# Performance work log

Hardware: AMD Instinct MI355X
Metric: run time of the kernel (lower is better)

## Reference

```python
import jax, jax.numpy as jnp
import numpy as np

N = 200000       # active voxels
C_IN = 64
C_OUT = 64
K = 3            # kernel size -> 27 offsets
BS = 2
SHAPE = (256, 256, 256)


def setup_inputs() -> dict:
    # unique active voxel coordinates (b, x, y, z)
    rng = np.random.default_rng(0)
    vol = SHAPE[0] * SHAPE[1] * SHAPE[2]
    lin = rng.choice(BS * vol, size=N, replace=False).astype(np.int64)
    b = lin // vol
    r = lin % vol
    x = r // (SHAPE[1] * SHAPE[2])
    r = r % (SHAPE[1] * SHAPE[2])
    y = r // SHAPE[2]
    z = r % SHAPE[2]
    coords = jnp.asarray(np.stack([b, x, y, z], axis=1).astype(np.int32))

    key = jax.random.key(0)
    k1, k2 = jax.random.split(key)
    features = jax.random.normal(k1, (N, C_IN), dtype=jnp.float32)
    # xavier_uniform over the full [K,K,K,C_in,C_out] kernel (bias init to 0, per module)
    fan_in, fan_out = 27 * C_IN, 27 * C_OUT
    limit = float(np.sqrt(6.0 / (fan_in + fan_out)))
    weight = jax.random.uniform(k2, (27, C_IN, C_OUT), dtype=jnp.float32,
                                minval=-limit, maxval=limit)
    bias = jnp.zeros((C_OUT,), dtype=jnp.float32)
    return {
        "features": features,
        "coords": coords,
        "weight": weight,
        "bias": bias,
        "spatial_shape": jnp.asarray(SHAPE, dtype=jnp.int32),
        "bs": BS,
    }


def _build_rulebook(coords, spatial_shape):
    """For every active site and each of the 27 offsets, find the index of the
    active neighbor at coord+offset, or n (invalid) if absent. Returns [27, n]."""
    n = coords.shape[0]
    X, Y, Z = spatial_shape[0], spatial_shape[1], spatial_shape[2]
    b, x, y, z = coords[:, 0], coords[:, 1], coords[:, 2], coords[:, 3]
    keys = ((b * X + x) * Y + y) * Z + z                      # [n] unique linear keys
    order = jnp.argsort(keys)
    skeys = keys[order]

    d = jnp.arange(-(K // 2), K // 2 + 1, dtype=jnp.int32)
    ox, oy, oz = jnp.meshgrid(d, d, d, indexing="ij")
    offs = jnp.stack([ox.ravel(), oy.ravel(), oz.ravel()], axis=1)  # [27,3]

    nxyz = coords[None, :, 1:4] + offs[:, None, :]            # [27,n,3]
    lim = jnp.stack([X, Y, Z]).astype(jnp.int32)
    inb = jnp.all((nxyz >= 0) & (nxyz < lim[None, None, :]), axis=-1)  # [27,n]
    qk = ((b[None, :] * X + nxyz[..., 0]) * Y + nxyz[..., 1]) * Z + nxyz[..., 2]

    pos = jnp.searchsorted(skeys, qk)                         # [27,n]
    posc = jnp.clip(pos, 0, n - 1)
    found = inb & (pos < n) & (skeys[posc] == qk)
    return jnp.where(found, order[posc], n)                   # n == padded zero row


def reference(features, coords, weight, bias, spatial_shape, bs):
    n = features.shape[0]
    idx = _build_rulebook(coords, spatial_shape)              # [27,n]
    feats_pad = jnp.concatenate(
        [features, jnp.zeros((1, features.shape[1]), features.dtype)], axis=0)

    def step(acc, xk):
        idx_k, w_k = xk
        # gather-GEMM-scatter for one kernel offset (submanifold: out sites = in sites)
        return acc + feats_pad[idx_k] @ w_k, None

    init = jnp.broadcast_to(bias.astype(features.dtype), (n, weight.shape[2]))
    out, _ = jax.lax.scan(step, init, (idx, weight))
    return out
```

## Files before the change

kernel.cpp:

```cpp
#include <hip/hip_runtime.h>
#include <cstdint>
#include <cstddef>


typedef __attribute__((ext_vector_type(8))) short bf16x8;
typedef __attribute__((ext_vector_type(4))) float f32x4;

static constexpr unsigned long long EMPTY64 = ~0ull;
static constexpr int LCAP = 512;
static constexpr unsigned NREGION = 27;
static constexpr unsigned CPAD = 16;
static constexpr int PB = 48;
static constexpr int NBWORDS = (2 << 24) >> 5;

__device__ __forceinline__ unsigned hash_mix(unsigned key) {
    unsigned h = key * 0x9E3779B1u;
    h ^= h >> 15;
    return h;
}

__device__ __forceinline__ unsigned short f2bf(float x) {
    unsigned u = __builtin_bit_cast(unsigned, x);
    return (unsigned short)((u + 0x7FFFu + ((u >> 16) & 1u)) >> 16);
}

__global__ void init_table_kernel(unsigned long long* __restrict__ table,
                                  int nslots, unsigned* __restrict__ bitmap,
                                  int nbwords, unsigned* __restrict__ cnts,
                                  const float* __restrict__ weight,
                                  unsigned short* __restrict__ wfrag) {
    int i = blockIdx.x * blockDim.x + threadIdx.x;
    if (i < nslots) table[i] = EMPTY64;
    if (i < nbwords) bitmap[i] = 0u;
    if (i < 512) {
        cnts[i] = 0u;
        const int lane = i & 63, nt = (i >> 6) & 3, ks = i >> 8;
        const float* __restrict__ w13 = weight + 13 * 4096;
        #pragma unroll
        for (int j = 0; j < 8; ++j) {
            const int k = ks * 32 + (lane >> 4) * 8 + j;
            const int n = nt * 16 + (lane & 15);
            wfrag[(size_t)i * 8 + j] = f2bf(w13[k * 64 + n]);
        }
    }
}

__global__ void insert_kernel(const int4* __restrict__ coords, int n,
                              unsigned long long* __restrict__ table,
                              unsigned mask, unsigned* __restrict__ bitmap) {
    int i = blockIdx.x * blockDim.x + threadIdx.x;
    if (i >= n) return;
    const int4 c = coords[i];
    const unsigned key = ((unsigned)c.x << 24) | ((unsigned)c.y << 16) |
                         ((unsigned)c.z << 8) | (unsigned)c.w;
    atomicOr(&bitmap[key >> 5], 1u << (key & 31));
    const unsigned long long entry =
        (unsigned long long)key | ((unsigned long long)(unsigned)i << 32);
    unsigned s = hash_mix(key) & mask;
    while (atomicCAS((unsigned long long*)&table[s], EMPTY64, entry) !=
           EMPTY64)
        s = (s + 1) & mask;
}

__global__ __launch_bounds__(512) void probe_pairs_kernel(
    const int4* __restrict__ coords, int n,
    const unsigned long long* __restrict__ table, unsigned mask,
    const unsigned* __restrict__ bitmap,
    unsigned* __restrict__ cnts, uint2* __restrict__ pairs, unsigned rcap)
{
    __shared__ unsigned lcnt;
    __shared__ unsigned lk[32], lkb[32], lkp[32];
    __shared__ uint2 lbuf[LCAP];
    if (threadIdx.x == 0) lcnt = 0u;
    if (threadIdx.x < 32) lk[threadIdx.x] = 0u;
    __syncthreads();

    const int site = blockIdx.x * blockDim.x + threadIdx.x;
    if (site < n) {
        const int4 c = coords[site];
        const int z = c.w;
        const int r = z & 31;

        unsigned lo[5], ex[5];
        #pragma unroll
        for (int g = 0; g < 5; ++g) {
            const int dx = (g < 3) ? -1 : 0;
            const int dy = (g < 3) ? (g - 1) : (g - 4);
            const int nx = c.y + dx, ny = c.z + dy;
            const bool rv = (((nx | ny) & ~255) == 0);
            const int q = ((((c.x << 8) | (nx & 255)) << 8) | (ny & 255)) << 8 | z;
            const int wq = q >> 5;
            lo[g] = rv ? bitmap[wq] : 0u;
            ex[g] = (rv && r == 31) ? bitmap[wq + 1]
                  : ((rv && r == 0 && wq > 0) ? bitmap[wq - 1] : 0u);
        }

        const unsigned zmask =
            ((z == 0) ? ~1u : ~0u) & ((z == 255) ? ~4u : ~0u);
        unsigned hitm = 0u;
        #pragma unroll
        for (int g = 0; g < 5; ++g) {
            unsigned tri;
            if (r == 0)        tri = ((lo[g] & 3u) << 1) | (ex[g] >> 31);
            else if (r == 31)  tri = ((lo[g] >> 30) & 3u) | ((ex[g] & 1u) << 2);
            else               tri = (lo[g] >> (r - 1)) & 7u;
            tri &= zmask;
            if (g == 4) tri &= 1u;
            hitm |= tri << (3 * g);
        }

        while (hitm) {
            const int b = __ffs(hitm) - 1;
            hitm &= hitm - 1;
            const int g = b / 3, d = b % 3;
            const int dx = (g < 3) ? -1 : 0;
            const int dy = (g < 3) ? (g - 1) : (g - 4);
            const int k = 3 * g + d;
            const unsigned key = ((unsigned)c.x << 24) |
                                 ((unsigned)(c.y + dx) << 16) |
                                 ((unsigned)(c.z + dy) << 8) |
                                 (unsigned)(z + d - 1);
            unsigned s = hash_mix(key) & mask;
            unsigned long long e = table[s];
            while (e != EMPTY64 && (unsigned)e != key) {
                s = (s + 1) & mask;
                e = table[s];
            }
            if (e == EMPTY64) continue;
            const unsigned nbi = (unsigned)(e >> 32);
            const uint2 p0 = make_uint2((unsigned)site | ((unsigned)k << 18),
                                        nbi);
            const uint2 p1 = make_uint2(nbi | ((unsigned)(26 - k) << 18),
                                        (unsigned)site);
            const unsigned li = atomicAdd(&lcnt, 2u);
            if (li + 1 < (unsigned)LCAP) {
                lbuf[li] = p0;
                lbuf[li + 1] = p1;
            } else {
                const unsigned g0 = atomicAdd(&cnts[k * CPAD], 1u);
                if (g0 < rcap) pairs[(size_t)k * rcap + g0] = p0;
                const unsigned g1 = atomicAdd(&cnts[(26 - k) * CPAD], 1u);
                if (g1 < rcap) pairs[(size_t)(26 - k) * rcap + g1] = p1;
            }
        }
    }

    __syncthreads();
    const unsigned nloc = lcnt < (unsigned)LCAP ? lcnt : (unsigned)LCAP;
    for (unsigned i = threadIdx.x; i < nloc; i += blockDim.x)
        atomicAdd(&lk[lbuf[i].x >> 18], 1u);
    __syncthreads();
    if (threadIdx.x < NREGION) {
        const unsigned c = lk[threadIdx.x];
        lkb[threadIdx.x] = c ? atomicAdd(&cnts[threadIdx.x * CPAD], c) : 0u;
        lkp[threadIdx.x] = 0u;
    }
    __syncthreads();
    for (unsigned i = threadIdx.x; i < nloc; i += blockDim.x) {
        const uint2 e = lbuf[i];
        const unsigned kk = e.x >> 18;
        const unsigned pos = atomicAdd(&lkp[kk], 1u);
        const unsigned idx = lkb[kk] + pos;
        if (idx < rcap) pairs[(size_t)kk * rcap + idx] = e;
    }
}

__global__ __launch_bounds__(256) void conv_center_mfma(
    const float* __restrict__ feats, const unsigned short* __restrict__ wfrag,
    const float* __restrict__ bias, float* __restrict__ out, int n)
{
    const int lane = threadIdx.x & 63;
    const int wid = blockIdx.x * (blockDim.x >> 6) + (threadIdx.x >> 6);
    const int s0 = wid * 16;
    if (s0 >= n) return;

    bf16x8 bfrag[2][4];
    #pragma unroll
    for (int ks = 0; ks < 2; ++ks)
        #pragma unroll
        for (int nt = 0; nt < 4; ++nt)
            bfrag[ks][nt] = *reinterpret_cast<const bf16x8*>(
                wfrag + ((size_t)((ks * 4 + nt) * 64 + lane)) * 8);

    const int arow = s0 + (lane & 15);
    const bool vrow = arow < n;
    const float* __restrict__ fbase =
        feats + (size_t)(vrow ? arow : 0) * 64 + (lane >> 4) * 8;

    f32x4 acc[4] = {{0.f, 0.f, 0.f, 0.f}, {0.f, 0.f, 0.f, 0.f},
                    {0.f, 0.f, 0.f, 0.f}, {0.f, 0.f, 0.f, 0.f}};

    #pragma unroll
    for (int ks = 0; ks < 2; ++ks) {
        const f32x4 flo = *reinterpret_cast<const f32x4*>(fbase + ks * 32);
        const f32x4 fhi = *reinterpret_cast<const f32x4*>(fbase + ks * 32 + 4);
        bf16x8 afrag;
        afrag[0] = (short)f2bf(flo.x); afrag[1] = (short)f2bf(flo.y);
        afrag[2] = (short)f2bf(flo.z); afrag[3] = (short)f2bf(flo.w);
        afrag[4] = (short)f2bf(fhi.x); afrag[5] = (short)f2bf(fhi.y);
        afrag[6] = (short)f2bf(fhi.z); afrag[7] = (short)f2bf(fhi.w);
        #pragma unroll
        for (int nt = 0; nt < 4; ++nt)
            acc[nt] = __builtin_amdgcn_mfma_f32_16x16x32_bf16(
                afrag, bfrag[ks][nt], acc[nt], 0, 0, 0);
    }

    const int crow0 = s0 + (lane >> 4) * 4;
    const int col = lane & 15;
    #pragma unroll
    for (int nt = 0; nt < 4; ++nt) {
        const float bv = bias[nt * 16 + col];
        #pragma unroll
        for (int r = 0; r < 4; ++r) {
            const int sr = crow0 + r;
            if (sr < n)
                out[(size_t)sr * 64 + nt * 16 + col] = acc[nt][r] + bv;
        }
    }
}

__global__ __launch_bounds__(256) void conv_pairs_kernel(
    const float* __restrict__ feats, const float* __restrict__ weight,
    const uint2* __restrict__ pairs, const unsigned* __restrict__ cnts,
    unsigned rcap, float* __restrict__ out)
{
    const int lane = threadIdx.x & 63;
    int r = blockIdx.x / PB;
    r += (r >= 13);
    unsigned cnt = cnts[r * CPAD];
    if (cnt > rcap) cnt = rcap;
    if (cnt == 0) return;
    const uint2* __restrict__ rp = pairs + (size_t)r * rcap;
    const float* __restrict__ wk = weight + (size_t)r * 4096;
    const unsigned wloc = (blockIdx.x % PB) * 4 + (threadIdx.x >> 6);
    for (unsigned p = wloc; p < cnt; p += (unsigned)(PB * 4)) {
        const uint2 pr = rp[p];
        const unsigned site = pr.x & 0x3FFFFu;
        const unsigned nbi = pr.y;
        const float4* __restrict__ fr =
            reinterpret_cast<const float4*>(feats + (size_t)nbi * 64);
        float a0 = 0.f, a1 = 0.f, a2 = 0.f, a3 = 0.f;
        #pragma unroll
        for (int q = 0; q < 16; ++q) {
            const float4 f = fr[q];
            a0 = fmaf(f.x, wk[(4 * q + 0) * 64 + lane], a0);
            a1 = fmaf(f.y, wk[(4 * q + 1) * 64 + lane], a1);
            a2 = fmaf(f.z, wk[(4 * q + 2) * 64 + lane], a2);
            a3 = fmaf(f.w, wk[(4 * q + 3) * 64 + lane], a3);
        }
        atomicAdd(&out[(size_t)site * 64 + lane], (a0 + a1) + (a2 + a3));
    }
}

extern "C" void kernel_launch(void* const* d_in, const int* in_sizes, int n_in,
                              void* d_out, int out_size, void* d_ws, size_t ws_size,
                              hipStream_t stream) {
    const float* feats  = (const float*)d_in[0];
    const int4*  coords = (const int4*)d_in[1];
    const float* weight = (const float*)d_in[2];
    const float* bias   = (const float*)d_in[3];
    float* out = (float*)d_out;

    const int n = in_sizes[1] / 4;

    const bool big = ws_size >= ((size_t)16 << 20);
    const int nslots = big ? (1 << 19) : (1 << 18);
    const unsigned mask = (unsigned)(nslots - 1);
    const int nbclear = NBWORDS + 4;
    unsigned long long* table = (unsigned long long*)d_ws;
    unsigned* bitmap = (unsigned*)(table + nslots);
    unsigned* cnts = bitmap + nbclear;
    unsigned short* wfrag = (unsigned short*)((char*)cnts + 2048);
    uint2* pairs = (uint2*)((char*)wfrag + 8192);
    const size_t used = (size_t)nslots * 8 + (size_t)nbclear * 4 + 2048 + 8192;
    size_t cap_sz = (ws_size > used) ? (ws_size - used) / sizeof(uint2) : 0;
    if (cap_sz > (size_t)(4 << 20)) cap_sz = (size_t)(4 << 20);
    const unsigned rcap = (unsigned)(cap_sz / NREGION);

    {
        const int work = (nslots > nbclear) ? nslots : nbclear;
        int blocks = (work + 255) / 256;
        init_table_kernel<<<blocks, 256, 0, stream>>>(table, nslots, bitmap,
                                                      nbclear, cnts, weight,
                                                      wfrag);
    }
    {
        int blocks = (n + 255) / 256;
        insert_kernel<<<blocks, 256, 0, stream>>>(coords, n, table, mask,
                                                  bitmap);
    }
    {
        int blocks = (n + 511) / 512;
        probe_pairs_kernel<<<blocks, 512, 0, stream>>>(coords, n, table, mask,
                                                       bitmap, cnts, pairs,
                                                       rcap);
    }
    {
        int waves = (n + 15) / 16;
        int blocks = (waves + 3) / 4;
        conv_center_mfma<<<blocks, 256, 0, stream>>>(feats, wfrag, bias, out, n);
    }
    {
        conv_pairs_kernel<<<26 * PB, 256, 0, stream>>>(feats, weight, pairs,
                                                       cnts, rcap, out);
    }
}
```

Before: 99.40 us.

## Replace per-site neighbor probe with bitmap-word sweep for pair generation

The per-site probe kernel is replaced by one that scans every 32-bit word of the occupancy bitmap (about 1M words) and builds neighbor masks with word-level bit operations. For each matched pair it looks up both endpoints in the hash table, caching the center lookup across offsets. This removes the per-site coords read and per-site bitmap gathers. In exchange it launches threads over the whole bitmap, most of which hold empty words, and it adds a second hash lookup per pair.

```diff
diff --git a/kernel.cpp b/kernel.cpp
--- a/kernel.cpp
+++ b/kernel.cpp
@@ -22,6 +22,19 @@
 __device__ __forceinline__ unsigned short f2bf(float x) {
     unsigned u = __builtin_bit_cast(unsigned, x);
     return (unsigned short)((u + 0x7FFFu + ((u >> 16) & 1u)) >> 16);
+}
+
+__device__ __forceinline__ unsigned lookup_idx(
+    const unsigned long long* __restrict__ table, unsigned mask, unsigned key)
+{
+    unsigned s = hash_mix(key) & mask;
+    unsigned long long e = table[s];
+    while ((unsigned)e != key) {
+        if (e == EMPTY64) return 0xFFFFFFFFu;
+        s = (s + 1) & mask;
+        e = table[s];
+    }
+    return (unsigned)(e >> 32);
 }
 
 __global__ void init_table_kernel(unsigned long long* __restrict__ table,
@@ -62,10 +75,9 @@
         s = (s + 1) & mask;
 }
 
-__global__ __launch_bounds__(512) void probe_pairs_kernel(
-    const int4* __restrict__ coords, int n,
+__global__ __launch_bounds__(256) void probe_sweep_kernel(
     const unsigned long long* __restrict__ table, unsigned mask,
-    const unsigned* __restrict__ bitmap,
+    const unsigned* __restrict__ bitmap, int nwords,
     unsigned* __restrict__ cnts, uint2* __restrict__ pairs, unsigned rcap)
 {
     __shared__ unsigned lcnt;
@@ -75,72 +87,85 @@
     if (threadIdx.x < 32) lk[threadIdx.x] = 0u;
     __syncthreads();
 
-    const int site = blockIdx.x * blockDim.x + threadIdx.x;
-    if (site < n) {
-        const int4 c = coords[site];
-        const int z = c.w;
-        const int r = z & 31;
-
-        unsigned lo[5], ex[5];
-        #pragma unroll
-        for (int g = 0; g < 5; ++g) {
-            const int dx = (g < 3) ? -1 : 0;
-            const int dy = (g < 3) ? (g - 1) : (g - 4);
-            const int nx = c.y + dx, ny = c.z + dy;
-            const bool rv = (((nx | ny) & ~255) == 0);
-            const int q = ((((c.x << 8) | (nx & 255)) << 8) | (ny & 255)) << 8 | z;
-            const int wq = q >> 5;
-            lo[g] = rv ? bitmap[wq] : 0u;
-            ex[g] = (rv && r == 31) ? bitmap[wq + 1]
-                  : ((rv && r == 0 && wq > 0) ? bitmap[wq - 1] : 0u);
-        }
-
-        const unsigned zmask =
-            ((z == 0) ? ~1u : ~0u) & ((z == 255) ? ~4u : ~0u);
-        unsigned hitm = 0u;
-        #pragma unroll
-        for (int g = 0; g < 5; ++g) {
-            unsigned tri;
-            if (r == 0)        tri = ((lo[g] & 3u) << 1) | (ex[g] >> 31);
-            else if (r == 31)  tri = ((lo[g] >> 30) & 3u) | ((ex[g] & 1u) << 2);
-            else               tri = (lo[g] >> (r - 1)) & 7u;
-            tri &= zmask;
-            if (g == 4) tri &= 1u;
-            hitm |= tri << (3 * g);
-        }
-
-        while (hitm) {
-            const int b = __ffs(hitm) - 1;
-            hitm &= hitm - 1;
-            const int g = b / 3, d = b % 3;
-            const int dx = (g < 3) ? -1 : 0;
-            const int dy = (g < 3) ? (g - 1) : (g - 4);
-            const int k = 3 * g + d;
-            const unsigned key = ((unsigned)c.x << 24) |
-                                 ((unsigned)(c.y + dx) << 16) |
-                                 ((unsigned)(c.z + dy) << 8) |
-                                 (unsigned)(z + d - 1);
-            unsigned s = hash_mix(key) & mask;
-            unsigned long long e = table[s];
-            while (e != EMPTY64 && (unsigned)e != key) {
-                s = (s + 1) & mask;
-                e = table[s];
+    const int w = blockIdx.x * blockDim.x + threadIdx.x;
+    if (w < nwords) {
+        const unsigned cw = bitmap[w];
+        if (cw) {
+            const int zw = w & 7;
+            const int y = (w >> 3) & 255;
+            const int x = (w >> 11) & 255;
+            const bool needlo = (zw > 0) && (cw & 1u);
+            const bool needhi = (zw < 7) && (cw >> 31);
+
+            unsigned R[4], Rlo[4], Rhi[4];
+            #pragma unroll
+            for (int g = 0; g < 4; ++g) {
+                const int off = (g == 0) ? -2056 : (g == 1) ? -2048
+                              : (g == 2) ? -2040 : -8;
+                const bool vg = (g == 0) ? (x > 0 && y > 0)
+                              : (g == 1) ? (x > 0)
+                              : (g == 2) ? (x > 0 && y < 255)
+                              : (y > 0);
+                const int bwi = w + off;
+                R[g]   = vg ? bitmap[bwi] : 0u;
+                Rlo[g] = (vg && needlo) ? bitmap[bwi - 1] : 0u;
+                Rhi[g] = (vg && needhi) ? bitmap[bwi + 1] : 0u;
             }
-            if (e == EMPTY64) continue;
-            const unsigned nbi = (unsigned)(e >> 32);
-            const uint2 p0 = make_uint2((unsigned)site | ((unsigned)k << 18),
-                                        nbi);
-            const uint2 p1 = make_uint2(nbi | ((unsigned)(26 - k) << 18),
-                                        (unsigned)site);
-            const unsigned li = atomicAdd(&lcnt, 2u);
-            if (li + 1 < (unsigned)LCAP) {
-                lbuf[li] = p0;
-                lbuf[li + 1] = p1;
-            } else {
-                const unsigned g0 = atomicAdd(&cnts[k * CPAD], 1u);
-                if (g0 < rcap) pairs[(size_t)k * rcap + g0] = p0;
-                const unsigned g1 = atomicAdd(&cnts[(26 - k) * CPAD], 1u);
-                if (g1 < rcap) pairs[(size_t)(26 - k) * rcap + g1] = p1;
+            const unsigned Rl4 = needlo ? bitmap[w - 1] : 0u;
+
+            unsigned memo_key = 0xFFFFFFFFu, memo_site = 0u;
+            #pragma unroll
+            for (int g = 0; g < 5; ++g) {
+                const int dx = (g < 3) ? -1 : 0;
+                const int dy = (g < 3) ? (g - 1) : ((g == 3) ? -1 : 0);
+                unsigned pm[3];
+                if (g < 4) {
+                    pm[0] = cw & ((R[g] << 1) | (Rlo[g] >> 31));
+                    pm[1] = cw & R[g];
+                    pm[2] = cw & ((R[g] >> 1) | (Rhi[g] << 31));
+                } else {
+                    pm[0] = cw & ((cw << 1) | (Rl4 >> 31));
+                    pm[1] = 0u;
+                    pm[2] = 0u;
+                }
+                #pragma unroll
+                for (int d = 0; d < 3; ++d) {
+                    unsigned m = pm[d];
+                    const int k = 3 * g + d;
+                    const int duv = (dx << 16) + (dy << 8) + (d - 1);
+                    while (m) {
+                        const int p = __ffs(m) - 1;
+                        m &= m - 1;
+                        const unsigned vkey = ((unsigned)w << 5) | (unsigned)p;
+                        const unsigned ukey = (unsigned)((int)vkey + duv);
+                        unsigned site;
+                        if (vkey == memo_key) site = memo_site;
+                        else {
+                            site = lookup_idx(table, mask, vkey);
+                            memo_key = vkey; memo_site = site;
+                        }
+                        const unsigned nbi = lookup_idx(table, mask, ukey);
+                        if (site == 0xFFFFFFFFu || nbi == 0xFFFFFFFFu)
+                            continue;
+                        const uint2 p0 = make_uint2(
+                            site | ((unsigned)k << 18), nbi);
+                        const uint2 p1 = make_uint2(
+                            nbi | ((unsigned)(26 - k) << 18), site);
+                        const unsigned li = atomicAdd(&lcnt, 2u);
+                        if (li + 1 < (unsigned)LCAP) {
+                            lbuf[li] = p0;
+                            lbuf[li + 1] = p1;
+                        } else {
+                            const unsigned g0 =
+                                atomicAdd(&cnts[k * CPAD], 1u);
+                            if (g0 < rcap) pairs[(size_t)k * rcap + g0] = p0;
+                            const unsigned g1 =
+                                atomicAdd(&cnts[(26 - k) * CPAD], 1u);
+                            if (g1 < rcap)
+                                pairs[(size_t)(26 - k) * rcap + g1] = p1;
+                        }
+                    }
+                }
             }
         }
     }
@@ -290,9 +315,9 @@
                                                   bitmap);
     }
     {
-        int blocks = (n + 511) / 512;
-        probe_pairs_kernel<<<blocks, 512, 0, stream>>>(coords, n, table, mask,
-                                                       bitmap, cnts, pairs,
+        int blocks = (NBWORDS + 255) / 256;
+        probe_sweep_kernel<<<blocks, 256, 0, stream>>>(table, mask, bitmap,
+                                                       NBWORDS, cnts, pairs,
                                                        rcap);
     }
     {
```

After: 108.5 us. +9.2%, slower.

## Tile the occupancy bitmap as 4x8 y-z bricks for neighbor probing

Applied to the files above, without the earlier changes.

Changes the occupancy bitmap layout so each 32-bit word covers a 4(y) by 8(z) brick instead of 32 consecutive z values. Neighbor presence along the y and z offsets can then often be read from the same word, and the probe kernel is rewritten to build the 13-offset hit mask from brick words with explicit edge handling. The aim is fewer scattered bitmap loads per site in the rulebook probe, at the cost of more complex boundary logic and extra conditional loads at brick edges.

```diff
diff --git a/kernel.cpp b/kernel.cpp
--- a/kernel.cpp
+++ b/kernel.cpp
@@ -11,7 +11,7 @@
 static constexpr unsigned NREGION = 27;
 static constexpr unsigned CPAD = 16;
 static constexpr int PB = 48;
-static constexpr int NBWORDS = (2 << 24) >> 5;
+static constexpr int NBWORDS = 1 << 20;
 
 __device__ __forceinline__ unsigned hash_mix(unsigned key) {
     unsigned h = key * 0x9E3779B1u;
@@ -53,7 +53,10 @@
     const int4 c = coords[i];
     const unsigned key = ((unsigned)c.x << 24) | ((unsigned)c.y << 16) |
                          ((unsigned)c.z << 8) | (unsigned)c.w;
-    atomicOr(&bitmap[key >> 5], 1u << (key & 31));
+    const unsigned w = ((((unsigned)c.x << 8) | (unsigned)c.y) << 11) |
+                       (((unsigned)c.z >> 2) << 5) | ((unsigned)c.w >> 3);
+    const unsigned bit = (((unsigned)c.z & 3u) << 3) | ((unsigned)c.w & 7u);
+    atomicOr(&bitmap[w], 1u << bit);
     const unsigned long long entry =
         (unsigned long long)key | ((unsigned long long)(unsigned)i << 32);
     unsigned s = hash_mix(key) & mask;
@@ -78,53 +81,96 @@
     const int site = blockIdx.x * blockDim.x + threadIdx.x;
     if (site < n) {
         const int4 c = coords[site];
-        const int z = c.w;
-        const int r = z & 31;
-
-        unsigned lo[5], ex[5];
-        #pragma unroll
-        for (int g = 0; g < 5; ++g) {
+        const int b = c.x, x = c.y, y = c.z, z = c.w;
+        const int r = y & 3, yt = y >> 2;
+        const int s = z & 7, zt = z >> 3;
+        const bool redge = (r == 0) || (r == 3);
+        const int yta = (r == 0) ? yt - 1 : yt + 1;
+        const bool vya = (r == 0) ? (y > 0) : (y < 255);
+        const bool zl = (s == 0) && (z > 0);
+        const bool zh = (s == 7) && (z < 255);
+        const bool vxm = (x > 0);
+        const int xm = x - 1;
+
+        #define BWORD(xx, ytt, ztt) \
+            bitmap[((((unsigned)b << 8) | (unsigned)(xx)) << 11) | \
+                   ((unsigned)(ytt) << 5) | (unsigned)(ztt)]
+
+        const unsigned Pm  = vxm ? BWORD(xm, yt, zt) : 0u;
+        const unsigned Pa  = (vxm && redge && vya) ? BWORD(xm, yta, zt) : 0u;
+        const unsigned Pml = (vxm && zl) ? BWORD(xm, yt, zt - 1) : 0u;
+        const unsigned Pal = (vxm && redge && vya && zl)
+                                 ? BWORD(xm, yta, zt - 1) : 0u;
+        const unsigned Pmh = (vxm && zh) ? BWORD(xm, yt, zt + 1) : 0u;
+        const unsigned Pah = (vxm && redge && vya && zh)
+                                 ? BWORD(xm, yta, zt + 1) : 0u;
+        const unsigned Qm  = BWORD(x, yt, zt);
+        const bool qa = (r == 0) && (y > 0);
+        const unsigned Qa  = qa ? BWORD(x, yt - 1, zt) : 0u;
+        const unsigned Qml = zl ? BWORD(x, yt, zt - 1) : 0u;
+        const unsigned Qal = (qa && zl) ? BWORD(x, yt - 1, zt - 1) : 0u;
+        const unsigned Qmh = zh ? BWORD(x, yt, zt + 1) : 0u;
+        const unsigned Qah = (qa && zh) ? BWORD(x, yt - 1, zt + 1) : 0u;
+        #undef BWORD
+
+        const int rm1 = (r == 0) ? 3 : r - 1;
+        const int rp1 = (r == 3) ? 0 : r + 1;
+        const unsigned PA  = (r == 0) ? Pa : Pm;
+        const unsigned PAl = (r == 0) ? Pal : Pml;
+        const unsigned PAh = (r == 0) ? Pah : Pmh;
+        const unsigned PC  = (r == 3) ? Pa : Pm;
+        const unsigned PCl = (r == 3) ? Pal : Pml;
+        const unsigned PCh = (r == 3) ? Pah : Pmh;
+        const unsigned QA  = (r == 0) ? Qa : Qm;
+        const unsigned QAl = (r == 0) ? Qal : Qml;
+        const unsigned QAh = (r == 0) ? Qah : Qmh;
+
+        #define ROWB(W, rr) (((W) >> ((rr) * 8)) & 0xFFu)
+        unsigned triA, triB, triC, triD, bitE;
+        {
+            const unsigned cA = ROWB(PA, rm1), cB = ROWB(Pm, r),
+                           cC = ROWB(PC, rp1), cD = ROWB(QA, rm1),
+                           cE = ROWB(Qm, r);
+            if (s == 0) {
+                triA = ((cA & 3u) << 1) | (ROWB(PAl, rm1) >> 7);
+                triB = ((cB & 3u) << 1) | (ROWB(Pml, r)   >> 7);
+                triC = ((cC & 3u) << 1) | (ROWB(PCl, rp1) >> 7);
+                triD = ((cD & 3u) << 1) | (ROWB(QAl, rm1) >> 7);
+                bitE = ROWB(Qml, r) >> 7;
+            } else if (s == 7) {
+                triA = ((cA >> 6) & 3u) | ((ROWB(PAh, rm1) & 1u) << 2);
+                triB = ((cB >> 6) & 3u) | ((ROWB(Pmh, r)   & 1u) << 2);
+                triC = ((cC >> 6) & 3u) | ((ROWB(PCh, rp1) & 1u) << 2);
+                triD = ((cD >> 6) & 3u) | ((ROWB(QAh, rm1) & 1u) << 2);
+                bitE = (cE >> 6) & 1u;
+            } else {
+                triA = (cA >> (s - 1)) & 7u;
+                triB = (cB >> (s - 1)) & 7u;
+                triC = (cC >> (s - 1)) & 7u;
+                triD = (cD >> (s - 1)) & 7u;
+                bitE = (cE >> (s - 1)) & 1u;
+            }
+        }
+        #undef ROWB
+        unsigned hitm = triA | (triB << 3) | (triC << 6) | (triD << 9) |
+                        (bitE << 12);
+
+        while (hitm) {
+            const int bb = __ffs(hitm) - 1;
+            hitm &= hitm - 1;
+            const int g = bb / 3, d = bb % 3;
             const int dx = (g < 3) ? -1 : 0;
-            const int dy = (g < 3) ? (g - 1) : (g - 4);
-            const int nx = c.y + dx, ny = c.z + dy;
-            const bool rv = (((nx | ny) & ~255) == 0);
-            const int q = ((((c.x << 8) | (nx & 255)) << 8) | (ny & 255)) << 8 | z;
-            const int wq = q >> 5;
-            lo[g] = rv ? bitmap[wq] : 0u;
-            ex[g] = (rv && r == 31) ? bitmap[wq + 1]
-                  : ((rv && r == 0 && wq > 0) ? bitmap[wq - 1] : 0u);
-        }
-
-        const unsigned zmask =
-            ((z == 0) ? ~1u : ~0u) & ((z == 255) ? ~4u : ~0u);
-        unsigned hitm = 0u;
-        #pragma unroll
-        for (int g = 0; g < 5; ++g) {
-            unsigned tri;
-            if (r == 0)        tri = ((lo[g] & 3u) << 1) | (ex[g] >> 31);
-            else if (r == 31)  tri = ((lo[g] >> 30) & 3u) | ((ex[g] & 1u) << 2);
-            else               tri = (lo[g] >> (r - 1)) & 7u;
-            tri &= zmask;
-            if (g == 4) tri &= 1u;
-            hitm |= tri << (3 * g);
-        }
-
-        while (hitm) {
-            const int b = __ffs(hitm) - 1;
-            hitm &= hitm - 1;
-            const int g = b / 3, d = b % 3;
-            const int dx = (g < 3) ? -1 : 0;
-            const int dy = (g < 3) ? (g - 1) : (g - 4);
+            const int dy = (g < 3) ? (g - 1) : ((g == 3) ? -1 : 0);
             const int k = 3 * g + d;
-            const unsigned key = ((unsigned)c.x << 24) |
-                                 ((unsigned)(c.y + dx) << 16) |
-                                 ((unsigned)(c.z + dy) << 8) |
+            const unsigned key = ((unsigned)b << 24) |
+                                 ((unsigned)(x + dx) << 16) |
+                                 ((unsigned)(y + dy) << 8) |
                                  (unsigned)(z + d - 1);
-            unsigned s = hash_mix(key) & mask;
-            unsigned long long e = table[s];
+            unsigned sl = hash_mix(key) & mask;
+            unsigned long long e = table[sl];
             while (e != EMPTY64 && (unsigned)e != key) {
-                s = (s + 1) & mask;
-                e = table[s];
+                sl = (sl + 1) & mask;
+                e = table[sl];
             }
             if (e == EMPTY64) continue;
             const unsigned nbi = (unsigned)(e >> 32);
```

Result: no change. 97.76 us (-1.6%).
